# Kernel optimization log

Measured on AMD Instinct MI355X. Metric: run time of the kernel, lower is better.

The kernel has to match this reference:

```python
import jax, jax.numpy as jnp
import numpy as np

QUANT_RANGE = 8
HALF_RANGE = QUANT_RANGE // 2  # 4, i.e. int4-style symmetric clamp [-4, 3]


def _find_zero_scale(t):
    zero = t.min()
    scale = (t.max() - zero) / (2 * HALF_RANGE)
    return zero, scale


def _quantize(t):
    zero, scale = _find_zero_scale(t)
    q = jnp.clip((t - zero) / scale - HALF_RANGE, -HALF_RANGE, HALF_RANGE - 1).astype(jnp.int32)
    return q, zero, scale


def setup_inputs() -> dict:
    key = jax.random.key(0)
    k1, k2, k3 = jax.random.split(key, 3)
    in_features = 4096
    out_features = 4096
    batch = 4096  # must equal out_features (shift broadcast in original module)
    x = jax.random.normal(k1, (batch, in_features), dtype=jnp.float32)
    # kaiming_uniform_(a=sqrt(5)) -> bound = 1/sqrt(in_features)
    bound = 1.0 / np.sqrt(in_features)
    weight = jax.random.uniform(k2, (out_features, in_features), dtype=jnp.float32,
                                minval=-bound, maxval=bound)
    bias = jax.random.uniform(k3, (out_features,), dtype=jnp.float32,
                              minval=-bound, maxval=bound)
    return {"x": x, "weight": weight, "bias": bias}


def reference(x, weight, bias):
    # Quantize activations and weights with global affine (min/max) quant.
    x_q, zero_act, scale_act = _quantize(x)          # [B, in], scalars
    w_q, _, _ = _quantize(weight)                    # [out, in]
    # Integer-valued GEMM (done in fp32, matching F.linear on .float() casts).
    result = x_q.astype(jnp.float32) @ w_q.astype(jnp.float32).T + bias  # [B, out]
    # Dequantize with weight-row-sum shift.
    scale_weight = (weight.max() - weight.min()) / (2 * HALF_RANGE)
    weights_reduced = weight.sum(axis=1)             # [out]
    shift = (zero_act + HALF_RANGE * scale_act) * weights_reduced[:, None]  # [out, 1]
    # NOTE: original torch code broadcasts [B,out] + [out,1]; requires B == out.
    return result * scale_act * scale_weight + shift
```

## Files before the change

kernel.cpp:

```cpp
#include <hip/hip_runtime.h>
#include <stdint.h>


using i32x4  = __attribute__((ext_vector_type(4))) int;
using i32x16 = __attribute__((ext_vector_type(16))) int;

#define TID ((int)threadIdx.x)

__global__ __launch_bounds__(256) void k_stats(const float4* __restrict__ x,
                                               const float4* __restrict__ w,
                                               float* __restrict__ pmin,
                                               float* __restrict__ pmax,
                                               float* __restrict__ wsum) {
  const int blk = blockIdx.x;
  const bool isw = blk < 4096;
  const float4* src = isw ? (w + (size_t)blk * 1024)
                          : (x + (size_t)(blk - 4096) * 1024);
  float4 v0 = src[TID], v1 = src[256 + TID], v2 = src[512 + TID], v3 = src[768 + TID];
  float lmin = fminf(fminf(fminf(v0.x, v0.y), fminf(v0.z, v0.w)),
                     fminf(fminf(v1.x, v1.y), fminf(v1.z, v1.w)));
  lmin = fminf(lmin, fminf(fminf(fminf(v2.x, v2.y), fminf(v2.z, v2.w)),
                           fminf(fminf(v3.x, v3.y), fminf(v3.z, v3.w))));
  float lmax = fmaxf(fmaxf(fmaxf(v0.x, v0.y), fmaxf(v0.z, v0.w)),
                     fmaxf(fmaxf(v1.x, v1.y), fmaxf(v1.z, v1.w)));
  lmax = fmaxf(lmax, fmaxf(fmaxf(fmaxf(v2.x, v2.y), fmaxf(v2.z, v2.w)),
                           fmaxf(fmaxf(v3.x, v3.y), fmaxf(v3.z, v3.w))));
  float lsum = ((v0.x + v0.y) + (v0.z + v0.w)) + ((v1.x + v1.y) + (v1.z + v1.w)) +
               ((v2.x + v2.y) + (v2.z + v2.w)) + ((v3.x + v3.y) + (v3.z + v3.w));

#pragma unroll
  for (int d = 32; d > 0; d >>= 1) {
    lmin = fminf(lmin, __shfl_down(lmin, d));
    lmax = fmaxf(lmax, __shfl_down(lmax, d));
    lsum += __shfl_down(lsum, d);
  }
  __shared__ float smn[4], smx[4], ssm[4];
  const int wv = TID >> 6;
  if ((TID & 63) == 0) { smn[wv] = lmin; smx[wv] = lmax; ssm[wv] = lsum; }
  __syncthreads();
  if (TID == 0) {
    float mn = fminf(fminf(smn[0], smn[1]), fminf(smn[2], smn[3]));
    float mx = fmaxf(fmaxf(smx[0], smx[1]), fmaxf(smx[2], smx[3]));
    pmin[blk] = mn; pmax[blk] = mx;
    if (isw) wsum[blk] = (ssm[0] + ssm[1]) + (ssm[2] + ssm[3]);
  }
}

__global__ __launch_bounds__(256) void k_final(const float* __restrict__ pmin,
                                               const float* __restrict__ pmax,
                                               float* __restrict__ mmf) {
  float wmn = 1e30f, wmx = -1e30f, xmn = 1e30f, xmx = -1e30f;
  for (int i = TID; i < 4096; i += 256) {
    wmn = fminf(wmn, pmin[i]);        wmx = fmaxf(wmx, pmax[i]);
    xmn = fminf(xmn, pmin[4096 + i]); xmx = fmaxf(xmx, pmax[4096 + i]);
  }
#pragma unroll
  for (int d = 32; d > 0; d >>= 1) {
    xmn = fminf(xmn, __shfl_down(xmn, d));
    xmx = fmaxf(xmx, __shfl_down(xmx, d));
    wmn = fminf(wmn, __shfl_down(wmn, d));
    wmx = fmaxf(wmx, __shfl_down(wmx, d));
  }
  __shared__ float s[4][4];
  const int wv = TID >> 6;
  if ((TID & 63) == 0) { s[wv][0] = xmn; s[wv][1] = xmx; s[wv][2] = wmn; s[wv][3] = wmx; }
  __syncthreads();
  if (TID == 0) {
    mmf[0] = fminf(fminf(s[0][0], s[1][0]), fminf(s[2][0], s[3][0]));
    mmf[1] = fmaxf(fmaxf(s[0][1], s[1][1]), fmaxf(s[2][1], s[3][1]));
    mmf[2] = fminf(fminf(s[0][2], s[1][2]), fminf(s[2][2], s[3][2]));
    mmf[3] = fmaxf(fmaxf(s[0][3], s[1][3]), fmaxf(s[2][3], s[3][3]));
  }
}

__device__ __forceinline__ int q1i(float t, float zero, float scale) {
  float v = (t - zero) / scale - 4.0f;
  v = fminf(3.0f, fmaxf(-4.0f, v));
  return (int)v;
}

__device__ __forceinline__ unsigned pack4(float4 v, float zero, float scale) {
  return (q1i(v.x, zero, scale) & 255) | ((q1i(v.y, zero, scale) & 255) << 8) |
         ((q1i(v.z, zero, scale) & 255) << 16) | ((q1i(v.w, zero, scale) & 255) << 24);
}

__global__ __launch_bounds__(256) void k_quant(const float4* __restrict__ x,
                                               const float4* __restrict__ w,
                                               uint4* __restrict__ Xq,
                                               uint4* __restrict__ Wq,
                                               const float* __restrict__ mmf) {
  bool isx = (blockIdx.x < 4096);
  int row = isx ? blockIdx.x : (blockIdx.x - 4096);
  const float4* in = (isx ? x : w) + (size_t)row * 1024 + TID * 4;
  uint4* outq = (isx ? Xq : Wq) + (size_t)row * 256 + TID;
  float zero = isx ? mmf[0] : mmf[2];
  float scale = ((isx ? mmf[1] : mmf[3]) - zero) * 0.125f;
  float4 a = in[0], b = in[1], c = in[2], d = in[3];
  uint4 o;
  o.x = pack4(a, zero, scale);
  o.y = pack4(b, zero, scale);
  o.z = pack4(c, zero, scale);
  o.w = pack4(d, zero, scale);
  *outq = o;
}

__device__ __forceinline__ void gload_lds16(const char* g, char* l) {
  __builtin_amdgcn_global_load_lds(
      (__attribute__((address_space(1))) void*)(g),
      (__attribute__((address_space(3))) void*)(l), 16, 0, 0);
}

__global__ __launch_bounds__(512, 2) void k_gemm(const char* __restrict__ Xq,
                                                 const char* __restrict__ Wq,
                                                 const float* __restrict__ bias,
                                                 const float* __restrict__ wsum,
                                                 const float* __restrict__ mmf,
                                                 float* __restrict__ out) {
  __shared__ __align__(16) char LDS[131072];

  const int tid = TID;
  const int lane = tid & 63, wave = tid >> 6;
  const int c5 = lane & 31, h = lane >> 5;
  const int wm = (wave >> 2) * 128, wn = (wave & 3) * 64;

  const int bid = (int)blockIdx.x;
  const int swz = (bid & 7) * 32 + (bid >> 3);
  const int bx = swz & 15, by = swz >> 4;
  const int brow = by * 256, bcol = bx * 256;

  const int srow = tid >> 2;
  const int lcg = (tid & 3) ^ ((tid >> 3) & 3);
  const char* gA = Xq + (size_t)(brow + srow) * 4096 + lcg * 16;
  const char* gB = Wq + (size_t)(bcol + srow) * 4096 + lcg * 16;

  const int rsw = (c5 >> 1) & 3;

  i32x16 acc[4][2];
#pragma unroll
  for (int i = 0; i < 4; ++i)
#pragma unroll
    for (int j = 0; j < 2; ++j)
#pragma unroll
      for (int e = 0; e < 16; ++e) acc[i][j][e] = 0;

#pragma unroll
  for (int s = 0; s < 8; ++s) {
    const int kk = s >> 2, arr = (s >> 1) & 1, sh = s & 1;
    const char* gs = arr ? gB : gA;
    gload_lds16(gs + (size_t)kk * 64 + (size_t)sh * (128 * 4096),
                LDS + arr * 65536 + kk * 16384 + sh * 8192 + tid * 16);
  }
  asm volatile("s_waitcnt vmcnt(4)" ::: "memory");
  __builtin_amdgcn_s_barrier();

#pragma unroll 2
  for (int it = 0; it < 31; ++it) {
    const int cur = it & 1, nxt = cur ^ 1;
    const int curA = cur * 32768, curB = 65536 + cur * 32768;
    const int nxtA = nxt * 32768, nxtB = 65536 + nxt * 32768;
    const size_t kOff = (size_t)(2 * it + 2) * 64;
#pragma unroll
    for (int ph = 0; ph < 4; ++ph) {
      const int kk = ph >> 1, ktl = ph & 1;
      const int pco = ((ktl * 2 + h) ^ rsw) * 16;
      const int ab = curA + kk * 16384 + pco;
      const int bb = curB + kk * 16384 + pco;
      i32x4 af0 = *(const i32x4*)(LDS + ab + (wm + c5) * 64);
      i32x4 af1 = *(const i32x4*)(LDS + ab + (wm + 32 + c5) * 64);
      i32x4 af2 = *(const i32x4*)(LDS + ab + (wm + 64 + c5) * 64);
      i32x4 af3 = *(const i32x4*)(LDS + ab + (wm + 96 + c5) * 64);
      i32x4 bf0 = *(const i32x4*)(LDS + bb + (wn + c5) * 64);
      i32x4 bf1 = *(const i32x4*)(LDS + bb + (wn + 32 + c5) * 64);
      const char* gs = ktl ? gB : gA;
      char* ld = LDS + (ktl ? nxtB : nxtA) + kk * 16384 + tid * 16;
      gload_lds16(gs + kOff + (size_t)kk * 64, ld);
      gload_lds16(gs + kOff + (size_t)kk * 64 + (size_t)(128 * 4096), ld + 8192);
      if (ktl) asm volatile("s_waitcnt vmcnt(4)" ::: "memory");
      __builtin_amdgcn_s_barrier();
      asm volatile("s_waitcnt lgkmcnt(0)" ::: "memory");
      __builtin_amdgcn_sched_barrier(0);
      __builtin_amdgcn_s_setprio(1);
      acc[0][0] = __builtin_amdgcn_mfma_i32_32x32x32_i8(af0, bf0, acc[0][0], 0, 0, 0);
      acc[0][1] = __builtin_amdgcn_mfma_i32_32x32x32_i8(af0, bf1, acc[0][1], 0, 0, 0);
      acc[1][0] = __builtin_amdgcn_mfma_i32_32x32x32_i8(af1, bf0, acc[1][0], 0, 0, 0);
      acc[1][1] = __builtin_amdgcn_mfma_i32_32x32x32_i8(af1, bf1, acc[1][1], 0, 0, 0);
      acc[2][0] = __builtin_amdgcn_mfma_i32_32x32x32_i8(af2, bf0, acc[2][0], 0, 0, 0);
      acc[2][1] = __builtin_amdgcn_mfma_i32_32x32x32_i8(af2, bf1, acc[2][1], 0, 0, 0);
      acc[3][0] = __builtin_amdgcn_mfma_i32_32x32x32_i8(af3, bf0, acc[3][0], 0, 0, 0);
      acc[3][1] = __builtin_amdgcn_mfma_i32_32x32x32_i8(af3, bf1, acc[3][1], 0, 0, 0);
      __builtin_amdgcn_s_setprio(0);
      __builtin_amdgcn_s_barrier();
    }
  }

  asm volatile("s_waitcnt vmcnt(0)" ::: "memory");
  __builtin_amdgcn_s_barrier();
#pragma unroll
  for (int ph = 0; ph < 4; ++ph) {
    const int kk = ph >> 1, ktl = ph & 1;
    const int pco = ((ktl * 2 + h) ^ rsw) * 16;
    const int ab = 32768 + kk * 16384 + pco;
    const int bb = 98304 + kk * 16384 + pco;
    i32x4 af0 = *(const i32x4*)(LDS + ab + (wm + c5) * 64);
    i32x4 af1 = *(const i32x4*)(LDS + ab + (wm + 32 + c5) * 64);
    i32x4 af2 = *(const i32x4*)(LDS + ab + (wm + 64 + c5) * 64);
    i32x4 af3 = *(const i32x4*)(LDS + ab + (wm + 96 + c5) * 64);
    i32x4 bf0 = *(const i32x4*)(LDS + bb + (wn + c5) * 64);
    i32x4 bf1 = *(const i32x4*)(LDS + bb + (wn + 32 + c5) * 64);
    acc[0][0] = __builtin_amdgcn_mfma_i32_32x32x32_i8(af0, bf0, acc[0][0], 0, 0, 0);
    acc[0][1] = __builtin_amdgcn_mfma_i32_32x32x32_i8(af0, bf1, acc[0][1], 0, 0, 0);
    acc[1][0] = __builtin_amdgcn_mfma_i32_32x32x32_i8(af1, bf0, acc[1][0], 0, 0, 0);
    acc[1][1] = __builtin_amdgcn_mfma_i32_32x32x32_i8(af1, bf1, acc[1][1], 0, 0, 0);
    acc[2][0] = __builtin_amdgcn_mfma_i32_32x32x32_i8(af2, bf0, acc[2][0], 0, 0, 0);
    acc[2][1] = __builtin_amdgcn_mfma_i32_32x32x32_i8(af2, bf1, acc[2][1], 0, 0, 0);
    acc[3][0] = __builtin_amdgcn_mfma_i32_32x32x32_i8(af3, bf0, acc[3][0], 0, 0, 0);
    acc[3][1] = __builtin_amdgcn_mfma_i32_32x32x32_i8(af3, bf1, acc[3][1], 0, 0, 0);
  }

  float sa = (mmf[1] - mmf[0]) * 0.125f;
  float sw = (mmf[3] - mmf[2]) * 0.125f;
  float mid = mmf[0] + 4.0f * sa;

  const int col0 = bcol + wn + c5;
  const float b0 = bias[col0], b1 = bias[col0 + 32];
#pragma unroll
  for (int i = 0; i < 4; ++i) {
    const int rbase = brow + wm + i * 32 + 4 * h;
#pragma unroll
    for (int g = 0; g < 4; ++g) {
#pragma unroll
      for (int q = 0; q < 4; ++q) {
        const int row = rbase + 8 * g + q;
        const float shift = mid * wsum[row];
        float* po = out + (size_t)row * 4096 + col0;
        po[0]  = ((float)acc[i][0][g * 4 + q] + b0) * sa * sw + shift;
        po[32] = ((float)acc[i][1][g * 4 + q] + b1) * sa * sw + shift;
      }
    }
  }
}

extern "C" void kernel_launch(void* const* d_in, const int* in_sizes, int n_in,
                              void* d_out, int out_size, void* d_ws, size_t ws_size,
                              hipStream_t stream) {
  (void)in_sizes; (void)n_in; (void)out_size; (void)ws_size;
  const float* x = (const float*)d_in[0];
  const float* w = (const float*)d_in[1];
  const float* bias = (const float*)d_in[2];
  float* out = (float*)d_out;

  char* ws = (char*)d_ws;
  float* mmf = (float*)ws;
  float* wsum = (float*)(ws + 1024);
  float* pmin = (float*)(ws + 32768);
  float* pmax = (float*)(ws + 65536);
  char* Xq = ws + 131072;
  char* Wq = ws + 131072 + (size_t)16777216;

  k_stats<<<8192, 256, 0, stream>>>((const float4*)x, (const float4*)w, pmin, pmax, wsum);
  k_final<<<1, 256, 0, stream>>>(pmin, pmax, mmf);
  k_quant<<<8192, 256, 0, stream>>>((const float4*)x, (const float4*)w,
                                    (uint4*)Xq, (uint4*)Wq, mmf);
  k_gemm<<<256, 512, 0, stream>>>(Xq, Wq, bias, wsum, mmf, out);
}
```

Baseline: 247.7 us.

## Restructure int8 GEMM main loop to two barriers per iteration

Regroups the int8 MFMA main loop by K-chunk. Each chunk now issues all four global-to-LDS prefetches for A and B up front, then runs two MFMA k-steps, then does one vmcnt wait and one barrier. This replaces four phases per iteration, each with its own barrier pair, and drops the explicit lgkmcnt waits, sched_barrier and setprio. The aim is to cut synchronisation overhead and let the compiler interleave LDS reads with MFMAs. The cost is losing the hand-tuned priority and scheduling control. The prologue and epilogue are restructured to match.

```diff
diff --git a/kernel.cpp b/kernel.cpp
--- a/kernel.cpp
+++ b/kernel.cpp
@@ -144,11 +144,13 @@
       for (int e = 0; e < 16; ++e) acc[i][j][e] = 0;
 
 #pragma unroll
-  for (int s = 0; s < 8; ++s) {
-    const int kk = s >> 2, arr = (s >> 1) & 1, sh = s & 1;
-    const char* gs = arr ? gB : gA;
-    gload_lds16(gs + (size_t)kk * 64 + (size_t)sh * (128 * 4096),
-                LDS + arr * 65536 + kk * 16384 + sh * 8192 + tid * 16);
+  for (int kk = 0; kk < 2; ++kk) {
+    char* ldA = LDS + kk * 16384 + tid * 16;
+    char* ldB = LDS + 65536 + kk * 16384 + tid * 16;
+    gload_lds16(gA + (size_t)kk * 64, ldA);
+    gload_lds16(gA + (size_t)kk * 64 + (size_t)(128 * 4096), ldA + 8192);
+    gload_lds16(gB + (size_t)kk * 64, ldB);
+    gload_lds16(gB + (size_t)kk * 64 + (size_t)(128 * 4096), ldB + 8192);
   }
   asm volatile("s_waitcnt vmcnt(4)" ::: "memory");
   __builtin_amdgcn_s_barrier();
@@ -160,26 +162,53 @@
     const int nxtA = nxt * 32768, nxtB = 65536 + nxt * 32768;
     const size_t kOff = (size_t)(2 * it + 2) * 64;
 #pragma unroll
-    for (int ph = 0; ph < 4; ++ph) {
-      const int kk = ph >> 1, ktl = ph & 1;
-      const int pco = ((ktl * 2 + h) ^ rsw) * 16;
-      const int ab = curA + kk * 16384 + pco;
-      const int bb = curB + kk * 16384 + pco;
+    for (int kk = 0; kk < 2; ++kk) {
+      char* ldA = LDS + nxtA + kk * 16384 + tid * 16;
+      char* ldB = LDS + nxtB + kk * 16384 + tid * 16;
+      gload_lds16(gA + kOff + (size_t)kk * 64, ldA);
+      gload_lds16(gA + kOff + (size_t)kk * 64 + (size_t)(128 * 4096), ldA + 8192);
+      gload_lds16(gB + kOff + (size_t)kk * 64, ldB);
+      gload_lds16(gB + kOff + (size_t)kk * 64 + (size_t)(128 * 4096), ldB + 8192);
+
+#pragma unroll
+      for (int kt = 0; kt < 2; ++kt) {
+        const int pco = ((kt * 2 + h) ^ rsw) * 16;
+        const int ab = curA + kk * 16384 + pco;
+        const int bb = curB + kk * 16384 + pco;
+        i32x4 af0 = *(const i32x4*)(LDS + ab + (wm + c5) * 64);
+        i32x4 af1 = *(const i32x4*)(LDS + ab + (wm + 32 + c5) * 64);
+        i32x4 af2 = *(const i32x4*)(LDS + ab + (wm + 64 + c5) * 64);
+        i32x4 af3 = *(const i32x4*)(LDS + ab + (wm + 96 + c5) * 64);
+        i32x4 bf0 = *(const i32x4*)(LDS + bb + (wn + c5) * 64);
+        i32x4 bf1 = *(const i32x4*)(LDS + bb + (wn + 32 + c5) * 64);
+        acc[0][0] = __builtin_amdgcn_mfma_i32_32x32x32_i8(af0, bf0, acc[0][0], 0, 0, 0);
+        acc[0][1] = __builtin_amdgcn_mfma_i32_32x32x32_i8(af0, bf1, acc[0][1], 0, 0, 0);
+        acc[1][0] = __builtin_amdgcn_mfma_i32_32x32x32_i8(af1, bf0, acc[1][0], 0, 0, 0);
+        acc[1][1] = __builtin_amdgcn_mfma_i32_32x32x32_i8(af1, bf1, acc[1][1], 0, 0, 0);
+        acc[2][0] = __builtin_amdgcn_mfma_i32_32x32x32_i8(af2, bf0, acc[2][0], 0, 0, 0);
+        acc[2][1] = __builtin_amdgcn_mfma_i32_32x32x32_i8(af2, bf1, acc[2][1], 0, 0, 0);
+        acc[3][0] = __builtin_amdgcn_mfma_i32_32x32x32_i8(af3, bf0, acc[3][0], 0, 0, 0);
+        acc[3][1] = __builtin_amdgcn_mfma_i32_32x32x32_i8(af3, bf1, acc[3][1], 0, 0, 0);
+      }
+
+      asm volatile("s_waitcnt vmcnt(4)" ::: "memory");
+      __builtin_amdgcn_s_barrier();
+    }
+  }
+
+#pragma unroll
+  for (int kk = 0; kk < 2; ++kk) {
+#pragma unroll
+    for (int kt = 0; kt < 2; ++kt) {
+      const int pco = ((kt * 2 + h) ^ rsw) * 16;
+      const int ab = 32768 + kk * 16384 + pco;
+      const int bb = 98304 + kk * 16384 + pco;
       i32x4 af0 = *(const i32x4*)(LDS + ab + (wm + c5) * 64);
       i32x4 af1 = *(const i32x4*)(LDS + ab + (wm + 32 + c5) * 64);
       i32x4 af2 = *(const i32x4*)(LDS + ab + (wm + 64 + c5) * 64);
       i32x4 af3 = *(const i32x4*)(LDS + ab + (wm + 96 + c5) * 64);
       i32x4 bf0 = *(const i32x4*)(LDS + bb + (wn + c5) * 64);
       i32x4 bf1 = *(const i32x4*)(LDS + bb + (wn + 32 + c5) * 64);
-      const char* gs = ktl ? gB : gA;
-      char* ld = LDS + (ktl ? nxtB : nxtA) + kk * 16384 + tid * 16;
-      gload_lds16(gs + kOff + (size_t)kk * 64, ld);
-      gload_lds16(gs + kOff + (size_t)kk * 64 + (size_t)(128 * 4096), ld + 8192);
-      if (ktl) asm volatile("s_waitcnt vmcnt(4)" ::: "memory");
-      __builtin_amdgcn_s_barrier();
-      asm volatile("s_waitcnt lgkmcnt(0)" ::: "memory");
-      __builtin_amdgcn_sched_barrier(0);
-      __builtin_amdgcn_s_setprio(1);
       acc[0][0] = __builtin_amdgcn_mfma_i32_32x32x32_i8(af0, bf0, acc[0][0], 0, 0, 0);
       acc[0][1] = __builtin_amdgcn_mfma_i32_32x32x32_i8(af0, bf1, acc[0][1], 0, 0, 0);
       acc[1][0] = __builtin_amdgcn_mfma_i32_32x32x32_i8(af1, bf0, acc[1][0], 0, 0, 0);
@@ -188,33 +217,11 @@
       acc[2][1] = __builtin_amdgcn_mfma_i32_32x32x32_i8(af2, bf1, acc[2][1], 0, 0, 0);
       acc[3][0] = __builtin_amdgcn_mfma_i32_32x32x32_i8(af3, bf0, acc[3][0], 0, 0, 0);
       acc[3][1] = __builtin_amdgcn_mfma_i32_32x32x32_i8(af3, bf1, acc[3][1], 0, 0, 0);
-      __builtin_amdgcn_s_setprio(0);
+    }
+    if (kk == 0) {
+      asm volatile("s_waitcnt vmcnt(0)" ::: "memory");
       __builtin_amdgcn_s_barrier();
     }
-  }
-
-  asm volatile("s_waitcnt vmcnt(0)" ::: "memory");
-  __builtin_amdgcn_s_barrier();
-#pragma unroll
-  for (int ph = 0; ph < 4; ++ph) {
-    const int kk = ph >> 1, ktl = ph & 1;
-    const int pco = ((ktl * 2 + h) ^ rsw) * 16;
-    const int ab = 32768 + kk * 16384 + pco;
-    const int bb = 98304 + kk * 16384 + pco;
-    i32x4 af0 = *(const i32x4*)(LDS + ab + (wm + c5) * 64);
-    i32x4 af1 = *(const i32x4*)(LDS + ab + (wm + 32 + c5) * 64);
-    i32x4 af2 = *(const i32x4*)(LDS + ab + (wm + 64 + c5) * 64);
-    i32x4 af3 = *(const i32x4*)(LDS + ab + (wm + 96 + c5) * 64);
-    i32x4 bf0 = *(const i32x4*)(LDS + bb + (wn + c5) * 64);
-    i32x4 bf1 = *(const i32x4*)(LDS + bb + (wn + 32 + c5) * 64);
-    acc[0][0] = __builtin_amdgcn_mfma_i32_32x32x32_i8(af0, bf0, acc[0][0], 0, 0, 0);
-    acc[0][1] = __builtin_amdgcn_mfma_i32_32x32x32_i8(af0, bf1, acc[0][1], 0, 0, 0);
-    acc[1][0] = __builtin_amdgcn_mfma_i32_32x32x32_i8(af1, bf0, acc[1][0], 0, 0, 0);
-    acc[1][1] = __builtin_amdgcn_mfma_i32_32x32x32_i8(af1, bf1, acc[1][1], 0, 0, 0);
-    acc[2][0] = __builtin_amdgcn_mfma_i32_32x32x32_i8(af2, bf0, acc[2][0], 0, 0, 0);
-    acc[2][1] = __builtin_amdgcn_mfma_i32_32x32x32_i8(af2, bf1, acc[2][1], 0, 0, 0);
-    acc[3][0] = __builtin_amdgcn_mfma_i32_32x32x32_i8(af3, bf0, acc[3][0], 0, 0, 0);
-    acc[3][1] = __builtin_amdgcn_mfma_i32_32x32x32_i8(af3, bf1, acc[3][1], 0, 0, 0);
   }
 
   float sa = (mmf[1] - mmf[0]) * 0.125f;
```

Measured after the change: 248.5 us. Within noise of the previous version (+0.3%).
